# Kernel tuning notes

Measured on AMD Instinct MI355X. Metric: run time of the kernel, lower is better.

Reference implementation:

```python
import jax, jax.numpy as jnp
import numpy as np

DIM = 256


def _layernorm(x, g, b, eps=1e-5):
    mu = x.mean(-1, keepdims=True)
    var = x.var(-1, keepdims=True)  # biased, matches torch LayerNorm
    return (x - mu) / jnp.sqrt(var + eps) * g + b


def _softmax_kernel(d, proj, ratio, eps=1e-4):
    # FAVOR+ softmax kernel feature map: ratio*(exp(d@proj^T - |d|^2/2) + eps)
    dd = jnp.einsum('bnc,fc->bnf', d, proj)
    diag = 0.5 * jnp.sum(d * d, axis=-1, keepdims=True)
    return ratio * (jnp.exp(dd - diag) + eps)


def setup_inputs() -> dict:
    d = DIM
    rng = np.random.default_rng(0)
    # gaussian orthogonal random matrix (nb_features == dim -> single QR block)
    qmat, _ = np.linalg.qr(rng.standard_normal((d, d)))
    mult = np.linalg.norm(rng.standard_normal((d, d)), axis=1)
    proj = (np.diag(mult) @ qmat.T).astype(np.float32)

    key = jax.random.key(0)
    ks = jax.random.split(key, 8)

    def lin(k, o, i):
        s = 1.0 / np.sqrt(i)
        return jax.random.uniform(k, (o, i), jnp.float32, -s, s)

    return {
        'x': jax.random.normal(ks[0], (8, d, 64, 64), jnp.float32),
        'proj': jnp.asarray(proj),
        'wq': lin(ks[1], d, d), 'bq': jnp.zeros((d,), jnp.float32),
        'wk': lin(ks[2], d, d), 'bk': jnp.zeros((d,), jnp.float32),
        'wa': lin(ks[3], d, d), 'ba': jnp.zeros((d,), jnp.float32),
        'g1': jnp.ones((d,), jnp.float32), 'b1': jnp.zeros((d,), jnp.float32),
        'g2': jnp.ones((d,), jnp.float32), 'b2': jnp.zeros((d,), jnp.float32),
        'w1': lin(ks[4], 4 * d, d), 'fb1': jnp.zeros((4 * d,), jnp.float32),
        'w2': lin(ks[5], d, 4 * d), 'fb2': jnp.zeros((d,), jnp.float32),
    }


def reference(x, proj, wq, bq, wk, bk, wa, ba, g1, b1, g2, b2, w1, fb1, w2, fb2):
    B, C, H, W = x.shape
    N = H * W
    t = x.reshape(B, C, N).transpose(0, 2, 1)  # [B, N, C] tokens
    shortcut = t
    h = _layernorm(t, g1, b1)
    # 1x1 convs == per-token linears (conv weight [out,in,1,1] -> [out,in])
    q = h @ wq.T + bq
    k = h @ wk.T + bk
    v = h @ wa.T + ba
    # F.normalize(p=2, dim=channel, eps=5e-5): x / max(||x||, eps)
    qn = q / jnp.maximum(jnp.linalg.norm(q, axis=-1, keepdims=True), 5e-5)
    kn = k / jnp.maximum(jnp.linalg.norm(k, axis=-1, keepdims=True), 5e-5)
    ratio = proj.shape[0] ** -0.5
    qp = _softmax_kernel(qn, proj, ratio)  # [B, N, F]
    kp = _softmax_kernel(kn, proj, ratio)  # [B, N, F]
    # linear attention (single head, squeezed)
    k_sum = kp.sum(axis=1)                                    # [B, F]
    D_inv = 1.0 / jnp.einsum('bnf,bf->bn', qp, k_sum)         # [B, N]
    ctx = jnp.einsum('bnf,bnc->bfc', kp, v)                   # [B, F, C]
    out = jnp.einsum('bfc,bnf,bn->bnc', ctx, qp, D_inv)       # [B, N, C]
    t = shortcut + out
    h2 = _layernorm(t, g2, b2)
    m = jax.nn.gelu(h2 @ w1.T + fb1, approximate=False) @ w2.T + fb2
    t = t + m
    return t.transpose(0, 2, 1).reshape(B, C, H, W)
```

## Files before the change

### kernel.cpp

```cpp
#include <hip/hip_runtime.h>
#include <hip/hip_bf16.h>
#include <math.h>

typedef __hip_bfloat16 bf16;
typedef __attribute__((ext_vector_type(8))) short short8;
typedef __attribute__((ext_vector_type(4))) short short4v;
typedef __attribute__((ext_vector_type(4))) unsigned short ushort4v;
typedef __attribute__((ext_vector_type(4))) float f32x4;
typedef unsigned int u32;

#define BB 8
#define CC 256
#define NTOKB 4096
#define FF 256
#define HIDDEN 1024
#define NTOK (BB*NTOKB)

#if defined(__has_builtin)
#if __has_builtin(__builtin_amdgcn_global_load_lds)
#define HAS_GLL 1
#endif
#endif
#ifndef HAS_GLL
#define HAS_GLL 0
#endif

__device__ __forceinline__ float bf2f(bf16 x) { return __bfloat162float(x); }
__device__ __forceinline__ bf16 f2bf(float x) { return __float2bfloat16(x); }
__device__ __forceinline__ float clampf(float v, float lo, float hi) {
    return fminf(fmaxf(v, lo), hi);
}
__device__ __forceinline__ float s2f(short s) {
    unsigned int u = ((unsigned int)(unsigned short)s) << 16;
    float f; __builtin_memcpy(&f, &u, 4); return f;
}
__device__ __forceinline__ unsigned short f2bits(float v) {
    bf16 h = f2bf(v);
    unsigned short b; __builtin_memcpy(&b, &h, 2); return b;
}

#if HAS_GLL
__device__ __forceinline__ void gll16(const void* g, void* l) {
    __builtin_amdgcn_global_load_lds(
        (const __attribute__((address_space(1))) u32*)g,
        (__attribute__((address_space(3))) u32*)l, 16, 0, 0);
}
#endif

__device__ __forceinline__ float ldin(const void* p, size_t i, int fp32mode) {
    float v = fp32mode ? ((const float*)p)[i] : __bfloat162float(((const bf16*)p)[i]);
    if (!(v == v)) v = 0.f;
    return clampf(v, -1e4f, 1e4f);
}

__device__ __forceinline__ float wave_sum(float v) {
#pragma unroll
    for (int off = 32; off > 0; off >>= 1) v += __shfl_xor(v, off, 64);
    return v;
}

__global__ void detect_mode(const void* __restrict__ x, int* __restrict__ flag) {
    int i = threadIdx.x;
    float vb = __bfloat162float(((const bf16*)x)[(size_t)i * 37 + 1]);
    int bad = (!(vb == vb)) || (fabsf(vb) > 1e4f);
    unsigned long long m = __ballot(bad);
    if (i == 0) *flag = (m != 0ull) ? 1 : 0;
}

__global__ void convw_all(const void* __restrict__ wq, const void* __restrict__ wk,
                          const void* __restrict__ wa, const void* __restrict__ proj,
                          const void* __restrict__ w1, const void* __restrict__ w2,
                          bf16* __restrict__ dst, const int* __restrict__ mode) {
    int fp32 = *mode;
    int i = blockIdx.x * 256 + threadIdx.x;
    const void* src; size_t off;
    if (i < 262144) {
        int seg = i >> 16; off = (size_t)(i & 65535);
        src = seg == 0 ? wq : seg == 1 ? wk : seg == 2 ? wa : proj;
    } else if (i < 524288) { src = w1; off = (size_t)(i - 262144); }
    else { src = w2; off = (size_t)(i - 524288); }
    dst[i] = f2bf(ldin(src, off, fp32));
}


__global__ void transpose_in_off(const void* __restrict__ X, bf16* __restrict__ T,
                                 const int* __restrict__ mode, size_t eoff) {
    __shared__ float tile[32][33];
    int fp32 = *mode;
    int n0 = blockIdx.x * 32, c0 = blockIdx.y * 32;
    int tx = threadIdx.x, ty = threadIdx.y;
    for (int i = ty; i < 32; i += 8)
        tile[i][tx] = ldin(X, eoff + (size_t)(c0 + i) * NTOKB + n0 + tx, fp32);
    __syncthreads();
    for (int i = ty; i < 32; i += 8)
        T[(size_t)(n0 + i) * CC + c0 + tx] = f2bf(tile[tx][i]);
}

__global__ void transpose_out_off(const bf16* __restrict__ T, void* __restrict__ O,
                                  const int* __restrict__ mode, size_t eoff) {
    __shared__ float tile[32][33];
    int fp32 = *mode;
    int c0 = blockIdx.x * 32, n0 = blockIdx.y * 32;
    int tx = threadIdx.x, ty = threadIdx.y;
    for (int i = ty; i < 32; i += 8)
        tile[i][tx] = bf2f(T[(size_t)(n0 + i) * CC + c0 + tx]);
    __syncthreads();
    for (int i = ty; i < 32; i += 8) {
        size_t idx = eoff + (size_t)(c0 + i) * NTOKB + n0 + tx;
        float v = tile[tx][i];
        if (fp32) ((float*)O)[idx] = v; else ((bf16*)O)[idx] = f2bf(v);
    }
}

__global__ void transpose_in_z(const void* __restrict__ X, bf16* __restrict__ T,
                               const int* __restrict__ mode) {
    __shared__ float tile[32][33];
    int fp32 = *mode;
    int b = blockIdx.z;
    int n0 = blockIdx.x * 32, c0 = blockIdx.y * 32;
    int tx = threadIdx.x, ty = threadIdx.y;
    size_t eoff = (size_t)b * CC * NTOKB;
    for (int i = ty; i < 32; i += 8)
        tile[i][tx] = ldin(X, eoff + (size_t)(c0 + i) * NTOKB + n0 + tx, fp32);
    __syncthreads();
    for (int i = ty; i < 32; i += 8)
        T[((size_t)b * NTOKB + n0 + i) * CC + c0 + tx] = f2bf(tile[tx][i]);
}

__global__ void transpose_out_z(const bf16* __restrict__ T, void* __restrict__ O,
                                const int* __restrict__ mode) {
    __shared__ float tile[32][33];
    int fp32 = *mode;
    int b = blockIdx.z;
    int c0 = blockIdx.x * 32, n0 = blockIdx.y * 32;
    int tx = threadIdx.x, ty = threadIdx.y;
    for (int i = ty; i < 32; i += 8)
        tile[i][tx] = bf2f(T[((size_t)b * NTOKB + n0 + i) * CC + c0 + tx]);
    __syncthreads();
    for (int i = ty; i < 32; i += 8) {
        size_t idx = (size_t)b * CC * NTOKB + (size_t)(c0 + i) * NTOKB + n0 + tx;
        float v = tile[tx][i];
        if (fp32) ((float*)O)[idx] = v; else ((bf16*)O)[idx] = f2bf(v);
    }
}

__global__ void layernorm_k(const bf16* __restrict__ X, const void* __restrict__ g,
                            const void* __restrict__ bta, bf16* __restrict__ Y,
                            const int* __restrict__ mode) {
    int fp32 = *mode;
    int t = blockIdx.x * 4 + (threadIdx.x >> 6);
    int lane = threadIdx.x & 63;
    const bf16* row = X + (size_t)t * CC;
    float v[4], s = 0.f, s2 = 0.f;
#pragma unroll
    for (int j = 0; j < 4; j++) {
        v[j] = bf2f(row[lane + 64 * j]);
        s += v[j]; s2 += v[j] * v[j];
    }
    s = wave_sum(s); s2 = wave_sum(s2);
    float mu = s * (1.f / CC);
    float var = s2 * (1.f / CC) - mu * mu;
    float rstd = rsqrtf(fmaxf(var, 0.f) + 1e-5f);
    bf16* yrow = Y + (size_t)t * CC;
#pragma unroll
    for (int j = 0; j < 4; j++) {
        int c = lane + 64 * j;
        yrow[c] = f2bf((v[j] - mu) * rstd * ldin(g, c, fp32) + ldin(bta, c, fp32));
    }
}

__global__ void layernorm_v(const bf16* __restrict__ X, const void* __restrict__ g,
                            const void* __restrict__ bta, bf16* __restrict__ Y,
                            const int* __restrict__ mode) {
    int fp32 = *mode;
    int t = blockIdx.x * 4 + (threadIdx.x >> 6);
    int lane = threadIdx.x & 63;
    const short* row = (const short*)X + (size_t)t * CC;
    short4v u = *(const short4v*)&row[lane * 4];
    float v[4], s = 0.f, s2 = 0.f;
#pragma unroll
    for (int j = 0; j < 4; j++) { v[j] = s2f(u[j]); s += v[j]; s2 += v[j] * v[j]; }
    s = wave_sum(s); s2 = wave_sum(s2);
    float mu = s * (1.f / CC);
    float var = s2 * (1.f / CC) - mu * mu;
    float rstd = rsqrtf(fmaxf(var, 0.f) + 1e-5f);
    ushort4v o;
#pragma unroll
    for (int j = 0; j < 4; j++) {
        int c = lane * 4 + j;
        o[j] = f2bits((v[j] - mu) * rstd * ldin(g, c, fp32) + ldin(bta, c, fp32));
    }
    *(ushort4v*)((unsigned short*)Y + (size_t)t * CC + lane * 4) = o;
}

__global__ void rownorm_k(bf16* __restrict__ Q, float* __restrict__ DIAG) {
    int t = blockIdx.x * 4 + (threadIdx.x >> 6);
    int lane = threadIdx.x & 63;
    bf16* row = Q + (size_t)t * CC;
    float v[4], s2 = 0.f;
#pragma unroll
    for (int j = 0; j < 4; j++) { v[j] = bf2f(row[lane + 64 * j]); s2 += v[j] * v[j]; }
    s2 = wave_sum(s2);
    float nrm = sqrtf(fmaxf(s2, 0.f));
    float scale = 1.f / fmaxf(nrm, 5e-5f);
#pragma unroll
    for (int j = 0; j < 4; j++) row[lane + 64 * j] = f2bf(v[j] * scale);
    if (lane == 0) DIAG[t] = 0.5f * s2 * scale * scale;
}

__global__ void rownorm_v(bf16* __restrict__ Q, float* __restrict__ DIAG) {
    int t = blockIdx.x * 4 + (threadIdx.x >> 6);
    int lane = threadIdx.x & 63;
    short* row = (short*)Q + (size_t)t * CC;
    short4v u = *(const short4v*)&row[lane * 4];
    float v[4], s2 = 0.f;
#pragma unroll
    for (int j = 0; j < 4; j++) { v[j] = s2f(u[j]); s2 += v[j] * v[j]; }
    s2 = wave_sum(s2);
    float nrm = sqrtf(fmaxf(s2, 0.f));
    float scale = 1.f / fmaxf(nrm, 5e-5f);
    ushort4v o;
#pragma unroll
    for (int j = 0; j < 4; j++) o[j] = f2bits(v[j] * scale);
    *(ushort4v*)&row[lane * 4] = o;
    if (lane == 0) DIAG[t] = 0.5f * s2 * scale * scale;
}


template <int EPI>
__global__ void gemm_nt(const bf16* __restrict__ A, const void* __restrict__ Bw,
                        const void* __restrict__ bias, const float* __restrict__ diag,
                        const bf16* __restrict__ resid, bf16* __restrict__ Cm,
                        int M, int Nn, int Kk, const int* __restrict__ mode) {
    __shared__ float As[32][33];
    __shared__ float Bs[32][33];
    int fp32 = *mode;
    int tx = threadIdx.x, ty = threadIdx.y;
    int n0 = blockIdx.x * 32, m0 = blockIdx.y * 32;
    int tid = ty * 16 + tx;
    int lr = tid >> 5, lc = tid & 31;
    float acc[2][2] = {{0.f, 0.f}, {0.f, 0.f}};
    for (int k0 = 0; k0 < Kk; k0 += 32) {
#pragma unroll
        for (int i = 0; i < 4; i++) {
            int r = lr + 8 * i;
            As[r][lc] = bf2f(A[(size_t)(m0 + r) * Kk + k0 + lc]);
            Bs[r][lc] = ldin(Bw, (size_t)(n0 + r) * Kk + k0 + lc, fp32);
        }
        __syncthreads();
#pragma unroll
        for (int kk = 0; kk < 32; kk++) {
            float a0 = As[ty][kk], a1 = As[ty + 16][kk];
            float b0 = Bs[tx][kk], b1 = Bs[tx + 16][kk];
            acc[0][0] += a0 * b0; acc[0][1] += a0 * b1;
            acc[1][0] += a1 * b0; acc[1][1] += a1 * b1;
        }
        __syncthreads();
    }
#pragma unroll
    for (int i = 0; i < 2; i++)
#pragma unroll
        for (int j = 0; j < 2; j++) {
            int m = m0 + ty + 16 * i, n = n0 + tx + 16 * j;
            float v = acc[i][j];
            if (EPI == 0) {
                v = clampf(v + ldin(bias, n, fp32), -1e6f, 1e6f);
            } else if (EPI == 1) {
                v = fminf(0.0625f * (expf(fminf(v - diag[m], 60.f)) + 1e-4f), 1e8f);
            } else if (EPI == 2) {
                v += ldin(bias, n, fp32);
                v = 0.5f * v * (1.f + erff(v * 0.70710678118654752f));
            } else if (EPI == 3) {
                v += ldin(bias, n, fp32);
                v = clampf(v + bf2f(resid[(size_t)m * Nn + n]), -1e6f, 1e6f);
            }
            Cm[(size_t)m * Nn + n] = f2bf(v);
        }
}

__global__ void gemm_ctx_fb(const bf16* __restrict__ KP, const bf16* __restrict__ V,
                            float* __restrict__ CTX) {
    __shared__ float Ks[32][33];
    __shared__ float Vs[32][33];
    int c0 = blockIdx.x * 32, f0 = blockIdx.y * 32;
    int tx = threadIdx.x, ty = threadIdx.y;
    int tid = ty * 16 + tx, lr = tid >> 5, lc = tid & 31;
    float acc[2][2] = {{0.f, 0.f}, {0.f, 0.f}};
    for (int n0 = 0; n0 < NTOKB; n0 += 32) {
#pragma unroll
        for (int i = 0; i < 4; i++) {
            int r = lr + 8 * i;
            Ks[r][lc] = bf2f(KP[(size_t)(n0 + r) * FF + f0 + lc]);
            Vs[r][lc] = bf2f(V[(size_t)(n0 + r) * CC + c0 + lc]);
        }
        __syncthreads();
#pragma unroll
        for (int kk = 0; kk < 32; kk++) {
            float a0 = Ks[kk][ty], a1 = Ks[kk][ty + 16];
            float b0 = Vs[kk][tx], b1 = Vs[kk][tx + 16];
            acc[0][0] += a0 * b0; acc[0][1] += a0 * b1;
            acc[1][0] += a1 * b0; acc[1][1] += a1 * b1;
        }
        __syncthreads();
    }
#pragma unroll
    for (int i = 0; i < 2; i++)
#pragma unroll
        for (int j = 0; j < 2; j++)
            CTX[(size_t)(f0 + ty + 16 * i) * CC + c0 + tx + 16 * j] =
                clampf(acc[i][j], -1e18f, 1e18f);
}

__global__ void gemm_attnout_fb(const bf16* __restrict__ QP, const float* __restrict__ CTX,
                                const float* __restrict__ DINV, bf16* __restrict__ T) {
    __shared__ float As[32][33];
    __shared__ float Bs[32][33];
    int c0 = blockIdx.x * 32, m0 = blockIdx.y * 32;
    int tx = threadIdx.x, ty = threadIdx.y;
    int tid = ty * 16 + tx, lr = tid >> 5, lc = tid & 31;
    float acc[2][2] = {{0.f, 0.f}, {0.f, 0.f}};
    for (int k0 = 0; k0 < FF; k0 += 32) {
#pragma unroll
        for (int i = 0; i < 4; i++) {
            int r = lr + 8 * i;
            As[r][lc] = bf2f(QP[(size_t)(m0 + r) * FF + k0 + lc]);
            Bs[r][lc] = CTX[(size_t)(k0 + r) * CC + c0 + lc];
        }
        __syncthreads();
#pragma unroll
        for (int kk = 0; kk < 32; kk++) {
            float a0 = As[ty][kk], a1 = As[ty + 16][kk];
            float b0 = Bs[kk][tx], b1 = Bs[kk][tx + 16];
            acc[0][0] += a0 * b0; acc[0][1] += a0 * b1;
            acc[1][0] += a1 * b0; acc[1][1] += a1 * b1;
        }
        __syncthreads();
    }
#pragma unroll
    for (int i = 0; i < 2; i++)
#pragma unroll
        for (int j = 0; j < 2; j++) {
            int t = m0 + ty + 16 * i;
            size_t idx = (size_t)t * CC + c0 + tx + 16 * j;
            float addv = clampf(acc[i][j] * DINV[t], -1e6f, 1e6f);
            T[idx] = f2bf(bf2f(T[idx]) + addv);
        }
}

__global__ void colsum_k(const bf16* __restrict__ KP, float* __restrict__ KPART) {
    int chunk = blockIdx.x;
    int f = threadIdx.x;
    const bf16* base = KP + (size_t)chunk * 128 * FF + f;
    float acc = 0.f;
    for (int i = 0; i < 128; i++) acc += bf2f(base[(size_t)i * FF]);
    KPART[(size_t)chunk * FF + f] = acc;
}

__global__ void ksum_reduce(const float* __restrict__ KPART, float* __restrict__ KSUM) {
    int f = threadIdx.x;
    float acc = 0.f;
#pragma unroll
    for (int c = 0; c < 32; c++) acc += KPART[(size_t)c * FF + f];
    KSUM[f] = acc;
}

__global__ void dinv_k(const bf16* __restrict__ QP, const float* __restrict__ KSUM,
                       float* __restrict__ DINV) {
    int t = blockIdx.x * 4 + (threadIdx.x >> 6);
    int lane = threadIdx.x & 63;
    const bf16* row = QP + (size_t)t * FF;
    float s = 0.f;
#pragma unroll
    for (int j = 0; j < 4; j++) { int c = lane + 64 * j; s += bf2f(row[c]) * KSUM[c]; }
    s = wave_sum(s);
    if (lane == 0) DINV[t] = fminf(1.f / fmaxf(s, 1e-30f), 1e6f);
}

template <int BM, int BN, int EPI, bool TRANSC>
__global__ __launch_bounds__(256) void mgemm(
    const bf16* __restrict__ A, int lda, long long aZ,
    const void* __restrict__ Bv, int ldb, long long bZ,
    const void* __restrict__ bias, const float* __restrict__ diag,
    const float* __restrict__ dinv,
    bf16* __restrict__ Cb, int ldc, float* __restrict__ Cf,
    int MperZ, int Kc, int nchunk, const int* __restrict__ mode)
{
    constexpr int MI = BM / 32;
    constexpr int NI = BN / 32;
    __shared__ short As[BM][32];
    __shared__ short Bs[BN][32];
    int fp32 = *mode;
    int z = blockIdx.z;
    int bl = z / nchunk;
    int chunk = z - bl * nchunk;
    const short* Ag = (const short*)A + (size_t)bl * aZ;
    const short* Bg = (const short*)Bv + (size_t)bl * bZ;

    int bx = blockIdx.x, by = blockIdx.y;
    if ((gridDim.y & 7) == 0) {
        int NB = gridDim.x;
        int flat = by * NB + bx;
        int grp = flat / (8 * NB);
        int rem = flat - grp * 8 * NB;
        by = grp * 8 + (rem & 7);
        bx = rem >> 3;
    }
    int n0 = bx * BN, m0 = by * BM;

    int tid = threadIdx.x;
    int lane = tid & 63, wave = tid >> 6;
    int wm = wave >> 1, wn = wave & 1;
    int row16 = lane & 15, quad = lane >> 4;
    int lrow = lane >> 2, lcol = (lane & 3) * 8;

    f32x4 acc[MI][NI];
#pragma unroll
    for (int i = 0; i < MI; i++)
#pragma unroll
        for (int j = 0; j < NI; j++) acc[i][j] = {0.f, 0.f, 0.f, 0.f};

    int kBase = chunk * Kc;
    for (int kb = kBase; kb < kBase + Kc; kb += 32) {
#pragma unroll
        for (int t = 0; t < BM / 64; t++) {
            int rbase = wave * (BM / 4) + t * 16;
            const short* gsrc = &Ag[(size_t)(m0 + rbase + lrow) * lda + kb + lcol];
#if HAS_GLL
            gll16(gsrc, &As[rbase][0]);
#else
            *(short8*)&As[rbase + lrow][lcol] = *(const short8*)gsrc;
#endif
        }
#pragma unroll
        for (int t = 0; t < BN / 64; t++) {
            int rbase = wave * (BN / 4) + t * 16;
            const short* gsrc = &Bg[(size_t)(n0 + rbase + lrow) * ldb + kb + lcol];
#if HAS_GLL
            gll16(gsrc, &Bs[rbase][0]);
#else
            *(short8*)&Bs[rbase + lrow][lcol] = *(const short8*)gsrc;
#endif
        }
        __syncthreads();
        short8 af[MI], bfr[NI];
#pragma unroll
        for (int i = 0; i < MI; i++)
            af[i] = *(const short8*)&As[wm * (BM / 2) + i * 16 + row16][quad * 8];
#pragma unroll
        for (int j = 0; j < NI; j++)
            bfr[j] = *(const short8*)&Bs[wn * (BN / 2) + j * 16 + row16][quad * 8];
#pragma unroll
        for (int i = 0; i < MI; i++)
#pragma unroll
            for (int j = 0; j < NI; j++)
                acc[i][j] = __builtin_amdgcn_mfma_f32_16x16x32_bf16(af[i], bfr[j], acc[i][j], 0, 0, 0);
        __syncthreads();
    }

    float bv[NI];
    if (EPI == 0 || EPI == 2 || EPI == 3) {
#pragma unroll
        for (int j = 0; j < NI; j++)
            bv[j] = ldin(bias, n0 + wn * (BN / 2) + j * 16 + row16, fp32);
    } else {
#pragma unroll
        for (int j = 0; j < NI; j++) bv[j] = 0.f;
    }

#pragma unroll
    for (int i = 0; i < MI; i++) {
        int mb = m0 + wm * (BM / 2) + i * 16 + quad * 4;
        float dg[4] = {0.f, 0.f, 0.f, 0.f};
        if (EPI == 1) {
#pragma unroll
            for (int r = 0; r < 4; r++) dg[r] = diag[mb + r];
        }
        float dvv[4] = {0.f, 0.f, 0.f, 0.f};
        if (EPI == 5) {
#pragma unroll
            for (int r = 0; r < 4; r++) dvv[r] = dinv[(size_t)bl * MperZ + mb + r];
        }
#pragma unroll
        for (int j = 0; j < NI; j++) {
            int n = n0 + wn * (BN / 2) + j * 16 + row16;
            if (TRANSC) {
                ushort4v pack;
#pragma unroll
                for (int r = 0; r < 4; r++) {
                    float v = acc[i][j][r];
                    if (EPI == 0) {
                        v = clampf(v + bv[j], -1e6f, 1e6f);
                    } else {
                        v = fminf(0.0625f * (expf(fminf(v - dg[r], 60.f)) + 1e-4f), 1e8f);
                    }
                    pack[r] = f2bits(v);
                }
                int blq = mb >> 12, tb = mb & 4095;
                *(ushort4v*)((unsigned short*)Cb +
                    (size_t)blq * CC * NTOKB + (size_t)n * NTOKB + tb) = pack;
            } else {
#pragma unroll
                for (int r = 0; r < 4; r++) {
                    int m = mb + r;
                    float v = acc[i][j][r];
                    if (EPI == 0) {
                        v = clampf(v + bv[j], -1e6f, 1e6f);
                        Cb[(size_t)m * ldc + n] = f2bf(v);
                    } else if (EPI == 1) {
                        v = fminf(0.0625f * (expf(fminf(v - dg[r], 60.f)) + 1e-4f), 1e8f);
                        Cb[(size_t)m * ldc + n] = f2bf(v);
                    } else if (EPI == 2) {
                        v += bv[j];
                        v = 0.5f * v * (1.f + erff(v * 0.70710678118654752f));
                        Cb[(size_t)m * ldc + n] = f2bf(v);
                    } else if (EPI == 3) {
                        v += bv[j];
                        size_t idx = (size_t)m * ldc + n;
                        v = clampf(v + bf2f(Cb[idx]), -1e6f, 1e6f);
                        Cb[idx] = f2bf(v);
                    } else if (EPI == 4) {
                        Cf[(size_t)z * MperZ + (size_t)m * ldc + n] = v;
                    } else if (EPI == 5) {
                        size_t mg = (size_t)bl * MperZ + m;
                        float addv = clampf(v * dvv[r], -1e6f, 1e6f);
                        size_t idx = mg * ldc + n;
                        Cb[idx] = f2bf(bf2f(Cb[idx]) + addv);
                    }
                }
            }
        }
    }
}

__global__ void reduce_ctx(const float* __restrict__ PART, bf16* __restrict__ CTXT) {
    int f = blockIdx.x;
    int bl = blockIdx.y;
    int c = threadIdx.x;
    float s = 0.f;
#pragma unroll
    for (int ch = 0; ch < 8; ch++)
        s += PART[(((size_t)bl * 8 + ch) * FF + f) * CC + c];
    s = clampf(s, -1e18f, 1e18f);
    CTXT[((size_t)bl * CC + c) * FF + f] = f2bf(s);
}

__global__ void colsum_t(const bf16* __restrict__ KPT, float* __restrict__ KSUM) {
    int bl = blockIdx.y;
    int f = blockIdx.x * 4 + (threadIdx.x >> 6);
    int lane = threadIdx.x & 63;
    const short* row = (const short*)KPT + ((size_t)bl * FF + f) * NTOKB;
    float s = 0.f;
    for (int i = lane * 8; i < NTOKB; i += 512) {
        short8 v = *(const short8*)&row[i];
#pragma unroll
        for (int j = 0; j < 8; j++) s += s2f(v[j]);
    }
    s = wave_sum(s);
    if (lane == 0) KSUM[(size_t)bl * FF + f] = s;
}

__global__ void dinv_v(const bf16* __restrict__ QP, const float* __restrict__ KSUM,
                       float* __restrict__ DINV) {
    int bl = blockIdx.y;
    int t = blockIdx.x * 4 + (threadIdx.x >> 6);
    int lane = threadIdx.x & 63;
    const short* row = (const short*)QP + ((size_t)bl * NTOKB + t) * FF;
    const float* ks = KSUM + (size_t)bl * FF;
    short4v u = *(const short4v*)&row[lane * 4];
    float s = 0.f;
#pragma unroll
    for (int j = 0; j < 4; j++) s += s2f(u[j]) * ks[lane * 4 + j];
    s = wave_sum(s);
    if (lane == 0) DINV[(size_t)bl * NTOKB + t] = fminf(1.f / fmaxf(s, 1e-30f), 1e6f);
}

extern "C" void kernel_launch(void* const* d_in, const int* in_sizes, int n_in,
                              void* d_out, int out_size, void* d_ws, size_t ws_size,
                              hipStream_t stream) {
    const void* x    = d_in[0];
    const void* proj = d_in[1];
    const void* wq   = d_in[2];
    const void* bq   = d_in[3];
    const void* wk   = d_in[4];
    const void* bk   = d_in[5];
    const void* wa   = d_in[6];
    const void* ba   = d_in[7];
    const void* g1   = d_in[8];
    const void* b1   = d_in[9];
    const void* g2   = d_in[10];
    const void* b2   = d_in[11];
    const void* w1   = d_in[12];
    const void* fb1  = d_in[13];
    const void* w2   = d_in[14];
    const void* fb2  = d_in[15];

    char* base = (char*)d_ws;
    const size_t MB = 1048576ull;
    const bool fast = ws_size >= 160 * MB;

    if (fast) {
        bf16* T    = (bf16*)base;
        bf16* Hs   = (bf16*)(base + 16 * MB);
        bf16* Qs   = (bf16*)(base + 32 * MB);
        bf16* Ks   = (bf16*)(base + 48 * MB);
        bf16* VT   = (bf16*)(base + 64 * MB);
        bf16* MID  = (bf16*)(base + 80 * MB);
        float* PART = (float*)(base + 48 * MB);
        char* sm = base + 144 * MB;
        int* MODE = (int*)sm;
        float* DIAGQ = (float*)(sm + 1024);
        float* DIAGK = DIAGQ + NTOK;
        float* DINV  = DIAGK + NTOK;
        float* KSUM  = DINV + NTOK;
        bf16* CTXT   = (bf16*)(sm + 2 * MB);
        bf16* WB   = (bf16*)(base + 148 * MB);
        bf16* WQc  = WB;
        bf16* WKc  = WB + 65536;
        bf16* WAc  = WB + 131072;
        bf16* PRJc = WB + 196608;
        bf16* W1c  = WB + 262144;
        bf16* W2c  = WB + 524288;

        dim3 tb32(32, 8);
        detect_mode<<<1, 64, 0, stream>>>(x, MODE);
        convw_all<<<3072, 256, 0, stream>>>(wq, wk, wa, proj, w1, w2, WB, MODE);
        transpose_in_z<<<dim3(NTOKB / 32, CC / 32, BB), tb32, 0, stream>>>(x, T, MODE);

        layernorm_v<<<NTOK / 4, 256, 0, stream>>>(T, g1, b1, Hs, MODE);
        mgemm<128, 128, 0, false><<<dim3(2, 256, 1), 256, 0, stream>>>(
            Hs, 256, 0, WQc, 256, 0, bq, nullptr, nullptr, Qs, 256,
            nullptr, 0, 256, 1, MODE);
        mgemm<128, 128, 0, false><<<dim3(2, 256, 1), 256, 0, stream>>>(
            Hs, 256, 0, WKc, 256, 0, bk, nullptr, nullptr, Ks, 256,
            nullptr, 0, 256, 1, MODE);
        mgemm<128, 128, 0, true><<<dim3(2, 256, 1), 256, 0, stream>>>(
            Hs, 256, 0, WAc, 256, 0, ba, nullptr, nullptr, VT, 0,
            nullptr, 0, 256, 1, MODE);
        rownorm_v<<<NTOK / 4, 256, 0, stream>>>(Qs, DIAGQ);
        rownorm_v<<<NTOK / 4, 256, 0, stream>>>(Ks, DIAGK);
        mgemm<128, 128, 1, false><<<dim3(2, 256, 1), 256, 0, stream>>>(
            Qs, 256, 0, PRJc, 256, 0, nullptr, DIAGQ, nullptr, Hs, 256,
            nullptr, 0, 256, 1, MODE);
        mgemm<128, 128, 1, true><<<dim3(2, 256, 1), 256, 0, stream>>>(
            Ks, 256, 0, PRJc, 256, 0, nullptr, DIAGK, nullptr, Qs, 0,
            nullptr, 0, 256, 1, MODE);
        bf16* QP  = Hs;
        bf16* KPT = Qs;
        colsum_t<<<dim3(FF / 4, BB), 256, 0, stream>>>(KPT, KSUM);
        dinv_v<<<dim3(NTOKB / 4, BB), 256, 0, stream>>>(QP, KSUM, DINV);
        mgemm<64, 128, 4, false><<<dim3(2, 4, BB * 8), 256, 0, stream>>>(
            KPT, NTOKB, (long long)FF * NTOKB, VT, NTOKB, (long long)CC * NTOKB,
            nullptr, nullptr, nullptr, nullptr, CC,
            PART, FF * CC, 512, 8, MODE);
        reduce_ctx<<<dim3(FF, BB), 256, 0, stream>>>(PART, CTXT);
        mgemm<128, 128, 5, false><<<dim3(2, 32, BB), 256, 0, stream>>>(
            QP, 256, (long long)NTOKB * FF, CTXT, FF, (long long)CC * FF,
            nullptr, nullptr, DINV, T, 256,
            nullptr, NTOKB, 256, 1, MODE);
        layernorm_v<<<NTOK / 4, 256, 0, stream>>>(T, g2, b2, Hs, MODE);
        mgemm<128, 128, 2, false><<<dim3(8, 256, 1), 256, 0, stream>>>(
            Hs, 256, 0, W1c, 256, 0, fb1, nullptr, nullptr, MID, 1024,
            nullptr, 0, 256, 1, MODE);
        mgemm<128, 128, 3, false><<<dim3(2, 256, 1), 256, 0, stream>>>(
            MID, 1024, 0, W2c, 1024, 0, fb2, nullptr, nullptr, T, 256,
            nullptr, 0, 1024, 1, MODE);
        transpose_out_z<<<dim3(CC / 32, NTOKB / 32, BB), tb32, 0, stream>>>(T, d_out, MODE);
        return;
    }

    bf16* Tb   = (bf16*)(base);
    bf16* Hb   = (bf16*)(base + 2 * MB);
    bf16* Qb   = (bf16*)(base + 4 * MB);
    bf16* Kb   = (bf16*)(base + 6 * MB);
    bf16* Vb   = (bf16*)(base + 8 * MB);
    bf16* QPb  = (bf16*)(base + 2 * MB);
    bf16* KPb  = (bf16*)(base + 4 * MB);
    bf16* MIDb = (bf16*)(base + 2 * MB);
    bf16* H2b  = (bf16*)(base + 10 * MB);
    char* sm   = base + 12 * MB;
    int*   MODE  = (int*)sm;
    float* DIAGQ = (float*)(sm + 256);
    float* DIAGK = DIAGQ + NTOKB;
    float* DINV  = DIAGK + NTOKB;
    float* KSUM  = DINV + NTOKB;
    float* KPART = KSUM + FF;
    float* CTX   = KPART + 32 * FF;

    dim3 tb32(32, 8);
    dim3 tb16(16, 16);
    dim3 gq(CC / 32, NTOKB / 32);

    detect_mode<<<1, 64, 0, stream>>>(x, MODE);

    for (int b = 0; b < BB; b++) {
        size_t eoff = (size_t)b * CC * NTOKB;
        transpose_in_off<<<dim3(NTOKB / 32, CC / 32), tb32, 0, stream>>>(x, Tb, MODE, eoff);
        layernorm_k<<<NTOKB / 4, 256, 0, stream>>>(Tb, g1, b1, Hb, MODE);
        gemm_nt<0><<<gq, tb16, 0, stream>>>(Hb, wq, bq, nullptr, nullptr, Qb, NTOKB, CC, CC, MODE);
        gemm_nt<0><<<gq, tb16, 0, stream>>>(Hb, wk, bk, nullptr, nullptr, Kb, NTOKB, CC, CC, MODE);
        gemm_nt<0><<<gq, tb16, 0, stream>>>(Hb, wa, ba, nullptr, nullptr, Vb, NTOKB, CC, CC, MODE);
        rownorm_k<<<NTOKB / 4, 256, 0, stream>>>(Qb, DIAGQ);
        rownorm_k<<<NTOKB / 4, 256, 0, stream>>>(Kb, DIAGK);
        gemm_nt<1><<<gq, tb16, 0, stream>>>(Qb, proj, nullptr, DIAGQ, nullptr, QPb, NTOKB, FF, CC, MODE);
        gemm_nt<1><<<gq, tb16, 0, stream>>>(Kb, proj, nullptr, DIAGK, nullptr, KPb, NTOKB, FF, CC, MODE);
        colsum_k<<<32, 256, 0, stream>>>(KPb, KPART);
        ksum_reduce<<<1, 256, 0, stream>>>(KPART, KSUM);
        dinv_k<<<NTOKB / 4, 256, 0, stream>>>(QPb, KSUM, DINV);
        gemm_ctx_fb<<<dim3(CC / 32, FF / 32), tb16, 0, stream>>>(KPb, Vb, CTX);
        gemm_attnout_fb<<<gq, tb16, 0, stream>>>(QPb, CTX, DINV, Tb);
        layernorm_k<<<NTOKB / 4, 256, 0, stream>>>(Tb, g2, b2, H2b, MODE);
        gemm_nt<2><<<dim3(HIDDEN / 32, NTOKB / 32), tb16, 0, stream>>>(H2b, w1, fb1, nullptr, nullptr, MIDb, NTOKB, HIDDEN, CC, MODE);
        gemm_nt<3><<<gq, tb16, 0, stream>>>(MIDb, w2, fb2, nullptr, Tb, Tb, NTOKB, CC, HIDDEN, MODE);
        transpose_out_off<<<dim3(CC / 32, NTOKB / 32), tb32, 0, stream>>>(Tb, d_out, MODE, eoff);
    }
}
```

Before: 419.3 us.

## Fuse QKV and both FAVOR projections into batched GEMM launches, rebalance splits

Merges the three Q/K/V projection GEMMs into one launch with a 768-wide N dimension, routing each 256-column segment to its own output buffer (V stored transposed). The two random-feature projections for Q and K become one launch using the z dimension, with K features written transposed to a new dedicated buffer. The context GEMM's split-K goes from 8 to 16 chunks, and the final attention GEMM uses 128x64 tiles to launch more blocks. Biases are preconverted to float in the weight-conversion kernel. Together these cut launch count and raise occupancy, at the cost of a larger workspace requirement and a bigger partial-sum reduction.

```diff
diff --git a/kernel.cpp b/kernel.cpp
--- a/kernel.cpp
+++ b/kernel.cpp
@@ -70,16 +70,25 @@
 __global__ void convw_all(const void* __restrict__ wq, const void* __restrict__ wk,
                           const void* __restrict__ wa, const void* __restrict__ proj,
                           const void* __restrict__ w1, const void* __restrict__ w2,
-                          bf16* __restrict__ dst, const int* __restrict__ mode) {
+                          const void* __restrict__ bq, const void* __restrict__ bk,
+                          const void* __restrict__ ba,
+                          bf16* __restrict__ dst, float* __restrict__ bqkv,
+                          const int* __restrict__ mode) {
     int fp32 = *mode;
     int i = blockIdx.x * 256 + threadIdx.x;
-    const void* src; size_t off;
-    if (i < 262144) {
-        int seg = i >> 16; off = (size_t)(i & 65535);
-        src = seg == 0 ? wq : seg == 1 ? wk : seg == 2 ? wa : proj;
-    } else if (i < 524288) { src = w1; off = (size_t)(i - 262144); }
-    else { src = w2; off = (size_t)(i - 524288); }
-    dst[i] = f2bf(ldin(src, off, fp32));
+    if (i < 786432) {
+        const void* src; size_t off;
+        if (i < 262144) {
+            int seg = i >> 16; off = (size_t)(i & 65535);
+            src = seg == 0 ? wq : seg == 1 ? wk : seg == 2 ? wa : proj;
+        } else if (i < 524288) { src = w1; off = (size_t)(i - 262144); }
+        else { src = w2; off = (size_t)(i - 524288); }
+        dst[i] = f2bf(ldin(src, off, fp32));
+    } else if (i < 787200) {
+        int j = i - 786432;
+        const void* s = j < 256 ? bq : j < 512 ? bk : ba;
+        bqkv[j] = ldin(s, (size_t)(j & 255), fp32);
+    }
 }
 
 
@@ -382,7 +391,8 @@
     const void* __restrict__ Bv, int ldb, long long bZ,
     const void* __restrict__ bias, const float* __restrict__ diag,
     const float* __restrict__ dinv,
-    bf16* __restrict__ Cb, int ldc, float* __restrict__ Cf,
+    bf16* __restrict__ Cb, int ldc,
+    bf16* __restrict__ Cb2, bf16* __restrict__ Cb3, float* __restrict__ Cf,
     int MperZ, int Kc, int nchunk, const int* __restrict__ mode)
 {
     constexpr int MI = BM / 32;
@@ -462,6 +472,10 @@
 #pragma unroll
         for (int j = 0; j < NI; j++)
             bv[j] = ldin(bias, n0 + wn * (BN / 2) + j * 16 + row16, fp32);
+    } else if (EPI == 6) {
+#pragma unroll
+        for (int j = 0; j < NI; j++)
+            bv[j] = diag[n0 + wn * (BN / 2) + j * 16 + row16];
     } else {
 #pragma unroll
         for (int j = 0; j < NI; j++) bv[j] = 0.f;
@@ -475,6 +489,10 @@
 #pragma unroll
             for (int r = 0; r < 4; r++) dg[r] = diag[mb + r];
         }
+        if (EPI == 7) {
+#pragma unroll
+            for (int r = 0; r < 4; r++) dg[r] = diag[(size_t)bl * MperZ + mb + r];
+        }
         float dvv[4] = {0.f, 0.f, 0.f, 0.f};
         if (EPI == 5) {
 #pragma unroll
@@ -483,7 +501,44 @@
 #pragma unroll
         for (int j = 0; j < NI; j++) {
             int n = n0 + wn * (BN / 2) + j * 16 + row16;
-            if (TRANSC) {
+            if (EPI == 6) {
+                int seg = n0 >> 8;
+                int c = n & 255;
+                if (seg == 2) {
+                    ushort4v pack;
+#pragma unroll
+                    for (int r = 0; r < 4; r++)
+                        pack[r] = f2bits(clampf(acc[i][j][r] + bv[j], -1e6f, 1e6f));
+                    int blq = mb >> 12, tb = mb & 4095;
+                    *(ushort4v*)((unsigned short*)Cb3 +
+                        (size_t)blq * CC * NTOKB + (size_t)c * NTOKB + tb) = pack;
+                } else {
+                    bf16* dst = seg ? Cb2 : Cb;
+#pragma unroll
+                    for (int r = 0; r < 4; r++) {
+                        float v = clampf(acc[i][j][r] + bv[j], -1e6f, 1e6f);
+                        dst[(size_t)(mb + r) * CC + c] = f2bf(v);
+                    }
+                }
+            } else if (EPI == 7) {
+                if (bl == 1) {
+                    ushort4v pack;
+#pragma unroll
+                    for (int r = 0; r < 4; r++) {
+                        float v = fminf(0.0625f * (expf(fminf(acc[i][j][r] - dg[r], 60.f)) + 1e-4f), 1e8f);
+                        pack[r] = f2bits(v);
+                    }
+                    int blq = mb >> 12, tb = mb & 4095;
+                    *(ushort4v*)((unsigned short*)Cb2 +
+                        (size_t)blq * CC * NTOKB + (size_t)n * NTOKB + tb) = pack;
+                } else {
+#pragma unroll
+                    for (int r = 0; r < 4; r++) {
+                        float v = fminf(0.0625f * (expf(fminf(acc[i][j][r] - dg[r], 60.f)) + 1e-4f), 1e8f);
+                        Cb[(size_t)(mb + r) * ldc + n] = f2bf(v);
+                    }
+                }
+            } else if (TRANSC) {
                 ushort4v pack;
 #pragma unroll
                 for (int r = 0; r < 4; r++) {
@@ -538,8 +593,8 @@
     int c = threadIdx.x;
     float s = 0.f;
 #pragma unroll
-    for (int ch = 0; ch < 8; ch++)
-        s += PART[(((size_t)bl * 8 + ch) * FF + f) * CC + c];
+    for (int ch = 0; ch < 16; ch++)
+        s += PART[(((size_t)bl * 16 + ch) * FF + f) * CC + c];
     s = clampf(s, -1e18f, 1e18f);
     CTXT[((size_t)bl * CC + c) * FF + f] = f2bf(s);
 }
@@ -596,7 +651,7 @@
 
     char* base = (char*)d_ws;
     const size_t MB = 1048576ull;
-    const bool fast = ws_size >= 160 * MB;
+    const bool fast = ws_size >= 168 * MB;
 
     if (fast) {
         bf16* T    = (bf16*)base;
@@ -604,66 +659,54 @@
         bf16* Qs   = (bf16*)(base + 32 * MB);
         bf16* Ks   = (bf16*)(base + 48 * MB);
         bf16* VT   = (bf16*)(base + 64 * MB);
-        bf16* MID  = (bf16*)(base + 80 * MB);
-        float* PART = (float*)(base + 48 * MB);
-        char* sm = base + 144 * MB;
+        bf16* KPT  = (bf16*)(base + 80 * MB);
+        bf16* MID  = (bf16*)(base + 96 * MB);
+        float* PART = (float*)(base + 96 * MB);
+        char* sm = base + 160 * MB;
         int* MODE = (int*)sm;
         float* DIAGQ = (float*)(sm + 1024);
         float* DIAGK = DIAGQ + NTOK;
         float* DINV  = DIAGK + NTOK;
         float* KSUM  = DINV + NTOK;
         bf16* CTXT   = (bf16*)(sm + 2 * MB);
-        bf16* WB   = (bf16*)(base + 148 * MB);
-        bf16* WQc  = WB;
-        bf16* WKc  = WB + 65536;
-        bf16* WAc  = WB + 131072;
-        bf16* PRJc = WB + 196608;
-        bf16* W1c  = WB + 262144;
-        bf16* W2c  = WB + 524288;
+        bf16* WB     = (bf16*)(sm + 4 * MB);
+        float* BQKV  = (float*)(sm + 6 * MB);
 
         dim3 tb32(32, 8);
         detect_mode<<<1, 64, 0, stream>>>(x, MODE);
-        convw_all<<<3072, 256, 0, stream>>>(wq, wk, wa, proj, w1, w2, WB, MODE);
+        convw_all<<<3075, 256, 0, stream>>>(wq, wk, wa, proj, w1, w2,
+                                            bq, bk, ba, WB, BQKV, MODE);
         transpose_in_z<<<dim3(NTOKB / 32, CC / 32, BB), tb32, 0, stream>>>(x, T, MODE);
 
         layernorm_v<<<NTOK / 4, 256, 0, stream>>>(T, g1, b1, Hs, MODE);
-        mgemm<128, 128, 0, false><<<dim3(2, 256, 1), 256, 0, stream>>>(
-            Hs, 256, 0, WQc, 256, 0, bq, nullptr, nullptr, Qs, 256,
-            nullptr, 0, 256, 1, MODE);
-        mgemm<128, 128, 0, false><<<dim3(2, 256, 1), 256, 0, stream>>>(
-            Hs, 256, 0, WKc, 256, 0, bk, nullptr, nullptr, Ks, 256,
-            nullptr, 0, 256, 1, MODE);
-        mgemm<128, 128, 0, true><<<dim3(2, 256, 1), 256, 0, stream>>>(
-            Hs, 256, 0, WAc, 256, 0, ba, nullptr, nullptr, VT, 0,
-            nullptr, 0, 256, 1, MODE);
+        mgemm<128, 128, 6, false><<<dim3(6, 256, 1), 256, 0, stream>>>(
+            Hs, 256, 0, WB, 256, 0, nullptr, BQKV, nullptr,
+            Qs, 256, Ks, VT, nullptr, 0, 256, 1, MODE);
         rownorm_v<<<NTOK / 4, 256, 0, stream>>>(Qs, DIAGQ);
         rownorm_v<<<NTOK / 4, 256, 0, stream>>>(Ks, DIAGK);
-        mgemm<128, 128, 1, false><<<dim3(2, 256, 1), 256, 0, stream>>>(
-            Qs, 256, 0, PRJc, 256, 0, nullptr, DIAGQ, nullptr, Hs, 256,
-            nullptr, 0, 256, 1, MODE);
-        mgemm<128, 128, 1, true><<<dim3(2, 256, 1), 256, 0, stream>>>(
-            Ks, 256, 0, PRJc, 256, 0, nullptr, DIAGK, nullptr, Qs, 0,
-            nullptr, 0, 256, 1, MODE);
-        bf16* QP  = Hs;
-        bf16* KPT = Qs;
+        mgemm<128, 128, 7, false><<<dim3(2, 256, 2), 256, 0, stream>>>(
+            Qs, 256, 8388608LL , WB + 196608, 256, 0,
+            nullptr, DIAGQ, nullptr,
+            Hs, 256, KPT, nullptr, nullptr, NTOK, 256, 1, MODE);
+        bf16* QP = Hs;
         colsum_t<<<dim3(FF / 4, BB), 256, 0, stream>>>(KPT, KSUM);
         dinv_v<<<dim3(NTOKB / 4, BB), 256, 0, stream>>>(QP, KSUM, DINV);
-        mgemm<64, 128, 4, false><<<dim3(2, 4, BB * 8), 256, 0, stream>>>(
+        mgemm<64, 128, 4, false><<<dim3(2, 4, BB * 16), 256, 0, stream>>>(
             KPT, NTOKB, (long long)FF * NTOKB, VT, NTOKB, (long long)CC * NTOKB,
-            nullptr, nullptr, nullptr, nullptr, CC,
-            PART, FF * CC, 512, 8, MODE);
+            nullptr, nullptr, nullptr,
+            nullptr, CC, nullptr, nullptr, PART, FF * CC, 256, 16, MODE);
         reduce_ctx<<<dim3(FF, BB), 256, 0, stream>>>(PART, CTXT);
-        mgemm<128, 128, 5, false><<<dim3(2, 32, BB), 256, 0, stream>>>(
+        mgemm<128, 64, 5, false><<<dim3(4, 32, BB), 256, 0, stream>>>(
             QP, 256, (long long)NTOKB * FF, CTXT, FF, (long long)CC * FF,
-            nullptr, nullptr, DINV, T, 256,
-            nullptr, NTOKB, 256, 1, MODE);
+            nullptr, nullptr, DINV,
+            T, 256, nullptr, nullptr, nullptr, NTOKB, 256, 1, MODE);
         layernorm_v<<<NTOK / 4, 256, 0, stream>>>(T, g2, b2, Hs, MODE);
         mgemm<128, 128, 2, false><<<dim3(8, 256, 1), 256, 0, stream>>>(
-            Hs, 256, 0, W1c, 256, 0, fb1, nullptr, nullptr, MID, 1024,
-            nullptr, 0, 256, 1, MODE);
+            Hs, 256, 0, WB + 262144, 256, 0, fb1, nullptr, nullptr,
+            MID, 1024, nullptr, nullptr, nullptr, 0, 256, 1, MODE);
         mgemm<128, 128, 3, false><<<dim3(2, 256, 1), 256, 0, stream>>>(
-            MID, 1024, 0, W2c, 1024, 0, fb2, nullptr, nullptr, T, 256,
-            nullptr, 0, 1024, 1, MODE);
+            MID, 1024, 0, WB + 524288, 1024, 0, fb2, nullptr, nullptr,
+            T, 256, nullptr, nullptr, nullptr, 0, 1024, 1, MODE);
         transpose_out_z<<<dim3(CC / 32, NTOKB / 32, BB), tb32, 0, stream>>>(T, d_out, MODE);
         return;
     }
```

After: 409.5 us. -2.3%, faster.
